# Optimization experiments

Hardware: AMD Instinct MI355X
Metric: run time of the kernel (lower is better)

The kernel has to match this reference:

```python
import jax, jax.numpy as jnp
import numpy as np

B, T = 64, 200
NUM_C2 = 2000
NUM_D = 1000
V = 128

# NOTE: Dropout layers are identity in eval mode; this reference implements eval-mode forward.

def setup_inputs() -> dict:
    key = jax.random.key(0)
    ks = jax.random.split(key, 19)
    s = 0.05
    def nrm(k, shape):
        return jax.random.normal(k, shape, jnp.float32) * s
    return {
        "c_seq": jax.random.randint(ks[0], (B, T), 0, NUM_C2),
        "d_seq": jax.random.randint(ks[1], (B, T), 0, NUM_D),
        "r_seq": (jax.random.uniform(ks[2], (B, T)) < 0.5).astype(jnp.float32),
        "D_emb": nrm(ks[3], (NUM_D, 1)),
        "v_d": nrm(ks[4], (V,)),
        "v_r": nrm(ks[5], (V,)),
        "v_c": nrm(ks[6], (V,)),
        "W_ih": nrm(ks[7], (3 * V, 2 * V)),
        "W_hh": nrm(ks[8], (3 * V, V)),
        "b_ih": nrm(ks[9], (3 * V,)),
        "b_hh": nrm(ks[10], (3 * V,)),
        "W1a": nrm(ks[11], (V, V)),
        "b1a": nrm(ks[12], (V,)),
        "W1b": nrm(ks[13], (1, V)),
        "b1b": nrm(ks[14], (1,)),
        "W2a": nrm(ks[15], (V, 3 * V)),
        "b2a": nrm(ks[16], (V,)),
        "W2b": nrm(ks[17], (1, V)),
        "b2b": nrm(ks[18], (1,)),
    }


def reference(c_seq, d_seq, r_seq, D_emb, v_d, v_r, v_c,
              W_ih, W_hh, b_ih, b_hh, W1a, b1a, W1b, b1b,
              W2a, b2a, W2b, b2b):
    gamma_seq = D_emb[d_seq]                 # [B,T,1]
    v_d_seq = gamma_seq * v_d                # [B,T,V]
    v_r_seq = r_seq[..., None] * v_r         # [B,T,V]
    x = jnp.concatenate([v_d_seq, v_r_seq], axis=-1)  # [B,T,2V]

    # --- GRU (PyTorch gate ordering r,z,n), h0 = 0 ---
    def gru_step(h, x_t):
        gi = x_t @ W_ih.T + b_ih
        gh = h @ W_hh.T + b_hh
        i_r, i_z, i_n = jnp.split(gi, 3, axis=-1)
        h_r, h_z, h_n = jnp.split(gh, 3, axis=-1)
        r = jax.nn.sigmoid(i_r + h_r)
        z = jax.nn.sigmoid(i_z + h_z)
        n = jnp.tanh(i_n + r * h_n)
        h_new = (1.0 - z) * n + z * h
        return h_new, h_new

    h0 = jnp.zeros((c_seq.shape[0], v_d.shape[0]), x.dtype)
    _, h_seq = jax.lax.scan(gru_step, h0, jnp.swapaxes(x, 0, 1))
    h_seq = jnp.swapaxes(h_seq, 0, 1)        # [B,T,V]

    # linear_1 (dropout = identity in eval)
    alpha_seq = (jax.nn.relu(h_seq @ W1a.T + b1a) @ W1b.T + b1b)[..., 0]  # [B,T]

    # --- sequential memory update over time ---
    def mem_step(C, inputs):
        c_t, vd_t, vr_t = inputs             # [B], [B,V], [B,V]
        beta = jnp.take_along_axis(C, c_t[:, None], axis=1)   # [B,1]
        vc = beta * v_c                       # [B,V]
        hh = jax.nn.relu(jnp.concatenate([vc, vd_t, vr_t], axis=-1) @ W2a.T + b2a)
        new_c = hh @ W2b.T + b2b              # [B,1]
        oh = jax.nn.one_hot(c_t, C.shape[1], dtype=C.dtype)   # [B,K]
        C_new = C * (1.0 - oh) + new_c * oh
        return C_new, C_new

    C0 = jnp.zeros((c_seq.shape[0], NUM_C2), x.dtype)
    _, C_seq = jax.lax.scan(
        mem_step, C0,
        (jnp.swapaxes(c_seq, 0, 1), jnp.swapaxes(v_d_seq, 0, 1), jnp.swapaxes(v_r_seq, 0, 1)))
    C_seq = jnp.swapaxes(C_seq, 0, 1)[..., None]   # [B,T,K,1]
    return alpha_seq, h_seq, C_seq
```

## Files before the change

### kernel.cpp

```cpp
#include <hip/hip_runtime.h>
#include <hip/hip_bf16.h>
#include <cstdint>

#define BB 64
#define TT 200
#define KN 2000
#define VV 128
#define NGRU 16

typedef __attribute__((ext_vector_type(8))) short bf16x8;
typedef __attribute__((ext_vector_type(4))) float f32x4;
typedef _Float16 half8 __attribute__((ext_vector_type(8)));


__device__ __forceinline__ float sigm(float x) {
    return __builtin_amdgcn_rcpf(1.f + __expf(-x));
}
__device__ __forceinline__ float tanh_f(float x) {
    float e = __expf(2.f * x);
    return 1.f - 2.f * __builtin_amdgcn_rcpf(e + 1.f);
}

__device__ __forceinline__ void soft_barrier() {
    asm volatile("s_waitcnt lgkmcnt(0)" ::: "memory");
    __builtin_amdgcn_s_barrier();
    __builtin_amdgcn_sched_barrier(0);
}

__global__ void pre_kernel(const float* __restrict__ v_d, const float* __restrict__ v_r,
                           const float* __restrict__ v_c, const float* __restrict__ W_ih,
                           const float* __restrict__ W2a, float* __restrict__ ws)
{
    int g = blockIdx.x * 256 + threadIdx.x;
    float* pd = ws;
    float* pr = ws + 384;
    float* uc = ws + 768;
    float* ud = ws + 896;
    float* ur = ws + 1024;
    if (g < 384) {
        float a = 0.f, b = 0.f;
        for (int k = 0; k < VV; ++k) {
            a = fmaf(W_ih[g * 256 + k], v_d[k], a);
            b = fmaf(W_ih[g * 256 + VV + k], v_r[k], b);
        }
        pd[g] = a; pr[g] = b;
    }
    if (g < VV) {
        float a = 0.f, b = 0.f, c = 0.f;
        for (int k = 0; k < VV; ++k) {
            a = fmaf(W2a[g * 384 + k], v_c[k], a);
            b = fmaf(W2a[g * 384 + VV + k], v_d[k], b);
            c = fmaf(W2a[g * 384 + 2 * VV + k], v_r[k], c);
        }
        uc[g] = a; ud[g] = b; ur[g] = c;
    }
}

__device__ __forceinline__ half8 load_cvt8h(const float* p) {
    float4 a = *(const float4*)p;
    float4 c = *(const float4*)(p + 4);
    half8 r;
    r[0] = (_Float16)a.x; r[1] = (_Float16)a.y; r[2] = (_Float16)a.z; r[3] = (_Float16)a.w;
    r[4] = (_Float16)c.x; r[5] = (_Float16)c.y; r[6] = (_Float16)c.z; r[7] = (_Float16)c.w;
    return r;
}

__global__ __launch_bounds__(512, 1) void fused_kernel(
    const int* __restrict__ c_seq, const int* __restrict__ d_seq,
    const float* __restrict__ r_seq, const float* __restrict__ D_emb,
    const float* __restrict__ Whh, const float* __restrict__ bih,
    const float* __restrict__ bhh, const float* __restrict__ W2b,
    const float* __restrict__ b2a, const float* __restrict__ b2b,
    const float* __restrict__ ws, float* __restrict__ C_out,
    float* __restrict__ h_out)
{
    __shared__ __align__(16) _Float16 H_half[16 * 136];
    __shared__ __align__(8) float gam4[TT * 4], r4[TT * 4];
    __shared__ __align__(16) float C[KN];
    __shared__ float gam_row[TT], r_row[TT], n_row[TT];
    __shared__ int c_row[TT + 1];

    int tid = threadIdx.x;

    if (blockIdx.x < NGRU) {
        int b0 = blockIdx.x * 4;
        const float* pd = ws;
        const float* pr = ws + 384;

        for (int i = tid; i < TT * 4; i += 512) {
            int t = i >> 2, rr = i & 3;
            gam4[i] = D_emb[d_seq[(b0 + rr) * TT + t]];
            r4[i] = r_seq[(b0 + rr) * TT + t];
        }
        for (int i = tid; i < 16 * 136; i += 512) H_half[i] = (_Float16)0.f;

        int wid = tid >> 6, l = tid & 63;
        int cl = l & 15, gq = l >> 4;
        int nn = wid * 16 + cl;

        const float* wr = Whh + (size_t)nn * VV + gq * 8;
        const float* wz = Whh + (size_t)(nn + 128) * VV + gq * 8;
        const float* wn = Whh + (size_t)(nn + 256) * VV + gq * 8;
        half8 br0 = load_cvt8h(wr),      br1 = load_cvt8h(wr + 32),
              br2 = load_cvt8h(wr + 64), br3 = load_cvt8h(wr + 96);
        half8 bz0 = load_cvt8h(wz),      bz1 = load_cvt8h(wz + 32),
              bz2 = load_cvt8h(wz + 64), bz3 = load_cvt8h(wz + 96);
        half8 bn0 = load_cvt8h(wn),      bn1 = load_cvt8h(wn + 32),
              bn2 = load_cvt8h(wn + 64), bn3 = load_cvt8h(wn + 96);

        float gr_pd = pd[nn],        gr_pr = pr[nn],        gr_b = bih[nn] + bhh[nn];
        float gz_pd = pd[nn + 128],  gz_pr = pr[nn + 128],  gz_b = bih[nn + 128] + bhh[nn + 128];
        float gn_pd = pd[nn + 256],  gn_pr = pr[nn + 256],  gn_b = bih[nn + 256];
        float gn_bh = bhh[nn + 256];

        float h0 = 0.f;
        __syncthreads();

        for (int t = 0; t < TT; ++t) {
            asm volatile("" : "+v"(br0), "+v"(br1), "+v"(br2), "+v"(br3),
                              "+v"(bz0), "+v"(bz1), "+v"(bz2), "+v"(bz3),
                              "+v"(bn0), "+v"(bn1), "+v"(bn2), "+v"(bn3));
            const int ab = cl * 136 + gq * 8;
            half8 a0 = *(const half8*)&H_half[ab];
            half8 a1 = *(const half8*)&H_half[ab + 32];
            half8 a2 = *(const half8*)&H_half[ab + 64];
            half8 a3 = *(const half8*)&H_half[ab + 96];
            float g1 = gam4[t * 4 + gq];
            float q1 = r4[t * 4 + gq];

            f32x4 accr = {0.f, 0.f, 0.f, 0.f};
            f32x4 accz = {0.f, 0.f, 0.f, 0.f};
            f32x4 accn = {0.f, 0.f, 0.f, 0.f};
            accr[0] = fmaf(g1, gr_pd, fmaf(q1, gr_pr, gr_b));
            accz[0] = fmaf(g1, gz_pd, fmaf(q1, gz_pr, gz_b));
            accn[0] = gn_bh;
            float gin0 = fmaf(g1, gn_pd, fmaf(q1, gn_pr, gn_b));

            accr = __builtin_amdgcn_mfma_f32_16x16x32_f16(a0, br0, accr, 0, 0, 0);
            accr = __builtin_amdgcn_mfma_f32_16x16x32_f16(a1, br1, accr, 0, 0, 0);
            accr = __builtin_amdgcn_mfma_f32_16x16x32_f16(a2, br2, accr, 0, 0, 0);
            accr = __builtin_amdgcn_mfma_f32_16x16x32_f16(a3, br3, accr, 0, 0, 0);
            accz = __builtin_amdgcn_mfma_f32_16x16x32_f16(a0, bz0, accz, 0, 0, 0);
            accz = __builtin_amdgcn_mfma_f32_16x16x32_f16(a1, bz1, accz, 0, 0, 0);
            accz = __builtin_amdgcn_mfma_f32_16x16x32_f16(a2, bz2, accz, 0, 0, 0);
            accz = __builtin_amdgcn_mfma_f32_16x16x32_f16(a3, bz3, accz, 0, 0, 0);
            accn = __builtin_amdgcn_mfma_f32_16x16x32_f16(a0, bn0, accn, 0, 0, 0);
            accn = __builtin_amdgcn_mfma_f32_16x16x32_f16(a1, bn1, accn, 0, 0, 0);
            accn = __builtin_amdgcn_mfma_f32_16x16x32_f16(a2, bn2, accn, 0, 0, 0);
            accn = __builtin_amdgcn_mfma_f32_16x16x32_f16(a3, bn3, accn, 0, 0, 0);

            {
                float rg0 = sigm(accr[0]);
                float zg0 = sigm(accz[0]);
                float ng0 = tanh_f(fmaf(rg0, accn[0], gin0));
                h0 = fmaf(1.f - zg0, ng0, zg0 * h0);
                h_out[((size_t)(b0 + gq) * TT + t) * VV + nn] = h0;
                H_half[(gq * 4) * 136 + nn] = (_Float16)h0;
            }
            soft_barrier();
        }
    } else {
        int b = blockIdx.x - NGRU;
        const float* uc = ws + 768;
        const float* ud = ws + 896;
        const float* ur = ws + 1024;
        for (int i = tid; i < KN; i += 512) C[i] = 0.f;
        if (tid < TT) {
            gam_row[tid] = D_emb[d_seq[b * TT + tid]];
            r_row[tid] = r_seq[b * TT + tid];
            c_row[tid] = c_seq[b * TT + tid];
        }
        if (tid == 0) c_row[TT] = 0;
        __syncthreads();

        if (tid < 64) {
            int l = tid;
            float uc0 = uc[l], uc1 = uc[l + 64];
            float ud0 = ud[l], ud1 = ud[l + 64];
            float ur0 = ur[l], ur1 = ur[l + 64];
            float ba0 = b2a[l], ba1 = b2a[l + 64];
            float wb0 = W2b[l], wb1 = W2b[l + 64];
            float bb = b2b[0];
            float beta = 0.f;
            int ct = c_row[0];
            for (int t = 0; t < TT; ++t) {
                int ct1 = c_row[t + 1];
                float cpref = C[ct1];
                float g = gam_row[t], rr = r_row[t];
                float hh0 = fmaxf(fmaf(beta, uc0, fmaf(g, ud0, fmaf(rr, ur0, ba0))), 0.f);
                float hh1 = fmaxf(fmaf(beta, uc1, fmaf(g, ud1, fmaf(rr, ur1, ba1))), 0.f);
                float p = fmaf(hh0, wb0, hh1 * wb1);
                #pragma unroll
                for (int m = 32; m > 0; m >>= 1) p += __shfl_xor(p, m);
                float nc = p + bb;
                if (l == 0) { C[ct] = nc; n_row[t] = nc; }
                beta = (ct1 == ct) ? nc : cpref;
                ct = ct1;
            }
        }
        __syncthreads();

        int k0 = tid * 4;
        if (k0 < KN) {
            float4 cur = {0.f, 0.f, 0.f, 0.f};
            float* cop = C_out + (size_t)b * TT * KN + k0;
            for (int t = 0; t < TT; ++t) {
                int c = c_row[t];
                unsigned d = (unsigned)(c - k0);
                if (d < 4u) {
                    float v = n_row[t];
                    cur.x = (d == 0u) ? v : cur.x;
                    cur.y = (d == 1u) ? v : cur.y;
                    cur.z = (d == 2u) ? v : cur.z;
                    cur.w = (d == 3u) ? v : cur.w;
                }
                *(float4*)(cop + (size_t)t * KN) = cur;
            }
        }
    }
}

__device__ __forceinline__ short f2bf(float f) {
    uint32_t u = __float_as_uint(f);
    u = (u + 0x7FFFu + ((u >> 16) & 1u)) >> 16;
    return (short)u;
}
__device__ __forceinline__ bf16x8 load_cvt8(const float* p) {
    float4 a = *(const float4*)p;
    float4 c = *(const float4*)(p + 4);
    bf16x8 r;
    r[0] = f2bf(a.x); r[1] = f2bf(a.y); r[2] = f2bf(a.z); r[3] = f2bf(a.w);
    r[4] = f2bf(c.x); r[5] = f2bf(c.y); r[6] = f2bf(c.z); r[7] = f2bf(c.w);
    return r;
}

__global__ void alpha_kernel(const float* __restrict__ h_seq, const float* __restrict__ W1a,
                             const float* __restrict__ b1a, const float* __restrict__ W1b,
                             const float* __restrict__ b1b, float* __restrict__ alpha)
{
    int wave = threadIdx.x >> 6;
    int lane = threadIdx.x & 63;
    int tile = blockIdx.x * 4 + wave;
    int rowbase = tile * 16;
    int rl = lane & 15, g = lane >> 4;
    const float* hp = h_seq + (size_t)(rowbase + rl) * VV + g * 8;
    bf16x8 a0 = load_cvt8(hp);
    bf16x8 a1 = load_cvt8(hp + 32);
    bf16x8 a2 = load_cvt8(hp + 64);
    bf16x8 a3 = load_cvt8(hp + 96);
    float p0 = 0.f, p1 = 0.f, p2 = 0.f, p3 = 0.f;
    float bb = b1b[0];
    #pragma unroll
    for (int jt = 0; jt < 8; ++jt) {
        int j = jt * 16 + rl;
        const float* wp = W1a + (size_t)j * VV + g * 8;
        f32x4 acc = {0.f, 0.f, 0.f, 0.f};
        acc = __builtin_amdgcn_mfma_f32_16x16x32_bf16(a0, load_cvt8(wp), acc, 0, 0, 0);
        acc = __builtin_amdgcn_mfma_f32_16x16x32_bf16(a1, load_cvt8(wp + 32), acc, 0, 0, 0);
        acc = __builtin_amdgcn_mfma_f32_16x16x32_bf16(a2, load_cvt8(wp + 64), acc, 0, 0, 0);
        acc = __builtin_amdgcn_mfma_f32_16x16x32_bf16(a3, load_cvt8(wp + 96), acc, 0, 0, 0);
        float bj = b1a[j], wj = W1b[j];
        p0 += fmaxf(acc[0] + bj, 0.f) * wj;
        p1 += fmaxf(acc[1] + bj, 0.f) * wj;
        p2 += fmaxf(acc[2] + bj, 0.f) * wj;
        p3 += fmaxf(acc[3] + bj, 0.f) * wj;
    }
    #pragma unroll
    for (int m = 1; m < 16; m <<= 1) {
        p0 += __shfl_xor(p0, m);
        p1 += __shfl_xor(p1, m);
        p2 += __shfl_xor(p2, m);
        p3 += __shfl_xor(p3, m);
    }
    if (rl == 0) {
        alpha[rowbase + g * 4 + 0] = p0 + bb;
        alpha[rowbase + g * 4 + 1] = p1 + bb;
        alpha[rowbase + g * 4 + 2] = p2 + bb;
        alpha[rowbase + g * 4 + 3] = p3 + bb;
    }
}

extern "C" void kernel_launch(void* const* d_in, const int* in_sizes, int n_in,
                              void* d_out, int out_size, void* d_ws, size_t ws_size,
                              hipStream_t stream)
{
    const int*   c_seq = (const int*)d_in[0];
    const int*   d_seq = (const int*)d_in[1];
    const float* r_seq = (const float*)d_in[2];
    const float* D_emb = (const float*)d_in[3];
    const float* v_d   = (const float*)d_in[4];
    const float* v_r   = (const float*)d_in[5];
    const float* v_c   = (const float*)d_in[6];
    const float* W_ih  = (const float*)d_in[7];
    const float* W_hh  = (const float*)d_in[8];
    const float* b_ih  = (const float*)d_in[9];
    const float* b_hh  = (const float*)d_in[10];
    const float* W1a   = (const float*)d_in[11];
    const float* b1a   = (const float*)d_in[12];
    const float* W1b   = (const float*)d_in[13];
    const float* b1b   = (const float*)d_in[14];
    const float* W2a   = (const float*)d_in[15];
    const float* b2a   = (const float*)d_in[16];
    const float* W2b   = (const float*)d_in[17];
    const float* b2b   = (const float*)d_in[18];

    float* out   = (float*)d_out;
    float* alpha = out;
    float* h_seq = out + 12800;
    float* C_out = out + 12800 + 1638400;
    float* ws    = (float*)d_ws;

    hipLaunchKernelGGL(pre_kernel, dim3(2), dim3(256), 0, stream,
                       v_d, v_r, v_c, W_ih, W2a, ws);
    hipLaunchKernelGGL(fused_kernel, dim3(NGRU + BB), dim3(512), 0, stream,
                       c_seq, d_seq, r_seq, D_emb, W_hh, b_ih, b_hh,
                       W2b, b2a, b2b, ws, C_out, h_seq);
    hipLaunchKernelGGL(alpha_kernel, dim3(200), dim3(256), 0, stream,
                       h_seq, W1a, b1a, W1b, b1b, alpha);
}
```

Measured before the change: 120.8 us.

## Fold precompute into fused kernel, use counter-based group sync, stage W1a in LDS

Removes the separate pre_kernel launch and has each block compute its W_ih and W2a projections inline. GRU blocks become 1024 threads carrying two independent 4-batch groups, with double-buffered hidden state and a per-group LDS atomic counter replacing the block-wide barrier. Memory blocks go to 1024 threads writing C in float2 chunks. The alpha kernel now stages W1a as bf16 in shared memory and runs 8 waves per block. The intent is to cut launch overhead and barrier cost. The trade-offs are redundant dot products in every block and spin-wait overhead.

```diff
diff --git a/kernel.cpp b/kernel.cpp
--- a/kernel.cpp
+++ b/kernel.cpp
@@ -6,13 +6,12 @@
 #define TT 200
 #define KN 2000
 #define VV 128
-#define NGRU 16
+#define NGRU 8
 
 typedef __attribute__((ext_vector_type(8))) short bf16x8;
 typedef __attribute__((ext_vector_type(4))) float f32x4;
 typedef _Float16 half8 __attribute__((ext_vector_type(8)));
 
-
 __device__ __forceinline__ float sigm(float x) {
     return __builtin_amdgcn_rcpf(1.f + __expf(-x));
 }
@@ -21,39 +20,17 @@
     return 1.f - 2.f * __builtin_amdgcn_rcpf(e + 1.f);
 }
 
-__device__ __forceinline__ void soft_barrier() {
-    asm volatile("s_waitcnt lgkmcnt(0)" ::: "memory");
-    __builtin_amdgcn_s_barrier();
-    __builtin_amdgcn_sched_barrier(0);
-}
-
-__global__ void pre_kernel(const float* __restrict__ v_d, const float* __restrict__ v_r,
-                           const float* __restrict__ v_c, const float* __restrict__ W_ih,
-                           const float* __restrict__ W2a, float* __restrict__ ws)
-{
-    int g = blockIdx.x * 256 + threadIdx.x;
-    float* pd = ws;
-    float* pr = ws + 384;
-    float* uc = ws + 768;
-    float* ud = ws + 896;
-    float* ur = ws + 1024;
-    if (g < 384) {
-        float a = 0.f, b = 0.f;
-        for (int k = 0; k < VV; ++k) {
-            a = fmaf(W_ih[g * 256 + k], v_d[k], a);
-            b = fmaf(W_ih[g * 256 + VV + k], v_r[k], b);
-        }
-        pd[g] = a; pr[g] = b;
-    }
-    if (g < VV) {
-        float a = 0.f, b = 0.f, c = 0.f;
-        for (int k = 0; k < VV; ++k) {
-            a = fmaf(W2a[g * 384 + k], v_c[k], a);
-            b = fmaf(W2a[g * 384 + VV + k], v_d[k], b);
-            c = fmaf(W2a[g * 384 + 2 * VV + k], v_r[k], c);
-        }
-        uc[g] = a; ud[g] = b; ur[g] = c;
-    }
+__device__ __forceinline__ float dot128(const float* __restrict__ a,
+                                        const float* __restrict__ b) {
+    float s0 = 0.f, s1 = 0.f, s2 = 0.f, s3 = 0.f;
+    #pragma unroll 8
+    for (int k = 0; k < 128; k += 4) {
+        float4 x = *(const float4*)(a + k);
+        float4 y = *(const float4*)(b + k);
+        s0 = fmaf(x.x, y.x, s0); s1 = fmaf(x.y, y.y, s1);
+        s2 = fmaf(x.z, y.z, s2); s3 = fmaf(x.w, y.w, s3);
+    }
+    return (s0 + s1) + (s2 + s3);
 }
 
 __device__ __forceinline__ half8 load_cvt8h(const float* p) {
@@ -65,17 +42,20 @@
     return r;
 }
 
-__global__ __launch_bounds__(512, 1) void fused_kernel(
+__global__ __launch_bounds__(1024, 1) void fused_kernel(
     const int* __restrict__ c_seq, const int* __restrict__ d_seq,
     const float* __restrict__ r_seq, const float* __restrict__ D_emb,
-    const float* __restrict__ Whh, const float* __restrict__ bih,
-    const float* __restrict__ bhh, const float* __restrict__ W2b,
-    const float* __restrict__ b2a, const float* __restrict__ b2b,
-    const float* __restrict__ ws, float* __restrict__ C_out,
+    const float* __restrict__ W_ih, const float* __restrict__ Whh,
+    const float* __restrict__ bih, const float* __restrict__ bhh,
+    const float* __restrict__ v_d, const float* __restrict__ v_r,
+    const float* __restrict__ v_c, const float* __restrict__ W2a,
+    const float* __restrict__ W2b, const float* __restrict__ b2a,
+    const float* __restrict__ b2b, float* __restrict__ C_out,
     float* __restrict__ h_out)
 {
-    __shared__ __align__(16) _Float16 H_half[16 * 136];
-    __shared__ __align__(8) float gam4[TT * 4], r4[TT * 4];
+    __shared__ __align__(16) _Float16 Hbuf[2][2][16 * 136];
+    __shared__ __align__(8) float gam4[2][TT * 4], r4[2][TT * 4];
+    __shared__ unsigned cnt[2];
     __shared__ __align__(16) float C[KN];
     __shared__ float gam_row[TT], r_row[TT], n_row[TT];
     __shared__ int c_row[TT + 1];
@@ -83,20 +63,24 @@
     int tid = threadIdx.x;
 
     if (blockIdx.x < NGRU) {
-        int b0 = blockIdx.x * 4;
-        const float* pd = ws;
-        const float* pr = ws + 384;
-
-        for (int i = tid; i < TT * 4; i += 512) {
-            int t = i >> 2, rr = i & 3;
-            gam4[i] = D_emb[d_seq[(b0 + rr) * TT + t]];
-            r4[i] = r_seq[(b0 + rr) * TT + t];
-        }
-        for (int i = tid; i < 16 * 136; i += 512) H_half[i] = (_Float16)0.f;
-
         int wid = tid >> 6, l = tid & 63;
+        int g = wid >> 3, wg = wid & 7;
         int cl = l & 15, gq = l >> 4;
-        int nn = wid * 16 + cl;
+        int nn = wg * 16 + cl;
+        int b0g = blockIdx.x * 8 + g * 4;
+        int brow = b0g + gq;
+
+        for (int i = tid; i < TT * 8; i += 1024) {
+            int grp = i >= TT * 4;
+            int w = i - grp * TT * 4;
+            int t = w >> 2, rr = w & 3;
+            int bb_ = blockIdx.x * 8 + grp * 4 + rr;
+            gam4[grp][t * 4 + rr] = D_emb[d_seq[bb_ * TT + t]];
+            r4[grp][t * 4 + rr] = r_seq[bb_ * TT + t];
+        }
+        for (int i = tid; i < 2 * 2 * 16 * 136; i += 1024)
+            ((_Float16*)Hbuf)[i] = (_Float16)0.f;
+        if (tid < 2) cnt[tid] = 0u;
 
         const float* wr = Whh + (size_t)nn * VV + gq * 8;
         const float* wz = Whh + (size_t)(nn + 128) * VV + gq * 8;
@@ -108,9 +92,15 @@
         half8 bn0 = load_cvt8h(wn),      bn1 = load_cvt8h(wn + 32),
               bn2 = load_cvt8h(wn + 64), bn3 = load_cvt8h(wn + 96);
 
-        float gr_pd = pd[nn],        gr_pr = pr[nn],        gr_b = bih[nn] + bhh[nn];
-        float gz_pd = pd[nn + 128],  gz_pr = pr[nn + 128],  gz_b = bih[nn + 128] + bhh[nn + 128];
-        float gn_pd = pd[nn + 256],  gn_pr = pr[nn + 256],  gn_b = bih[nn + 256];
+        float gr_pd = dot128(W_ih + (size_t)nn * 256, v_d);
+        float gr_pr = dot128(W_ih + (size_t)nn * 256 + 128, v_r);
+        float gz_pd = dot128(W_ih + (size_t)(nn + 128) * 256, v_d);
+        float gz_pr = dot128(W_ih + (size_t)(nn + 128) * 256 + 128, v_r);
+        float gn_pd = dot128(W_ih + (size_t)(nn + 256) * 256, v_d);
+        float gn_pr = dot128(W_ih + (size_t)(nn + 256) * 256 + 128, v_r);
+        float gr_b = bih[nn] + bhh[nn];
+        float gz_b = bih[nn + 128] + bhh[nn + 128];
+        float gn_b = bih[nn + 256];
         float gn_bh = bhh[nn + 256];
 
         float h0 = 0.f;
@@ -120,13 +110,16 @@
             asm volatile("" : "+v"(br0), "+v"(br1), "+v"(br2), "+v"(br3),
                               "+v"(bz0), "+v"(bz1), "+v"(bz2), "+v"(bz3),
                               "+v"(bn0), "+v"(bn1), "+v"(bn2), "+v"(bn3));
+            const _Float16* Hr = Hbuf[g][t & 1];
+            _Float16* Hw = Hbuf[g][(t & 1) ^ 1];
+
             const int ab = cl * 136 + gq * 8;
-            half8 a0 = *(const half8*)&H_half[ab];
-            half8 a1 = *(const half8*)&H_half[ab + 32];
-            half8 a2 = *(const half8*)&H_half[ab + 64];
-            half8 a3 = *(const half8*)&H_half[ab + 96];
-            float g1 = gam4[t * 4 + gq];
-            float q1 = r4[t * 4 + gq];
+            half8 a0 = *(const half8*)&Hr[ab];
+            half8 a1 = *(const half8*)&Hr[ab + 32];
+            half8 a2 = *(const half8*)&Hr[ab + 64];
+            half8 a3 = *(const half8*)&Hr[ab + 96];
+            float g1 = gam4[g][t * 4 + gq];
+            float q1 = r4[g][t * 4 + gq];
 
             f32x4 accr = {0.f, 0.f, 0.f, 0.f};
             f32x4 accz = {0.f, 0.f, 0.f, 0.f};
@@ -154,33 +147,46 @@
                 float zg0 = sigm(accz[0]);
                 float ng0 = tanh_f(fmaf(rg0, accn[0], gin0));
                 h0 = fmaf(1.f - zg0, ng0, zg0 * h0);
-                h_out[((size_t)(b0 + gq) * TT + t) * VV + nn] = h0;
-                H_half[(gq * 4) * 136 + nn] = (_Float16)h0;
+                h_out[((size_t)brow * TT + t) * VV + nn] = h0;
+                Hw[(gq * 4) * 136 + nn] = (_Float16)h0;
             }
-            soft_barrier();
+
+            asm volatile("s_waitcnt lgkmcnt(0)" ::: "memory");
+            if (l == 0)
+                __hip_atomic_fetch_add(&cnt[g], 1u, __ATOMIC_RELEASE,
+                                       __HIP_MEMORY_SCOPE_WORKGROUP);
+            unsigned tgt = 8u * (unsigned)(t + 1);
+            while (__hip_atomic_load(&cnt[g], __ATOMIC_ACQUIRE,
+                                     __HIP_MEMORY_SCOPE_WORKGROUP) < tgt) {}
+            __builtin_amdgcn_sched_barrier(0);
         }
     } else {
         int b = blockIdx.x - NGRU;
-        const float* uc = ws + 768;
-        const float* ud = ws + 896;
-        const float* ur = ws + 1024;
-        for (int i = tid; i < KN; i += 512) C[i] = 0.f;
+        for (int i = tid; i < KN; i += 1024) C[i] = 0.f;
         if (tid < TT) {
             gam_row[tid] = D_emb[d_seq[b * TT + tid]];
             r_row[tid] = r_seq[b * TT + tid];
             c_row[tid] = c_seq[b * TT + tid];
         }
         if (tid == 0) c_row[TT] = 0;
-        __syncthreads();
-
+        float uc0 = 0.f, uc1 = 0.f, ud0 = 0.f, ud1 = 0.f, ur0 = 0.f, ur1 = 0.f;
+        float ba0 = 0.f, ba1 = 0.f, wb0 = 0.f, wb1 = 0.f, bb = 0.f;
         if (tid < 64) {
             int l = tid;
-            float uc0 = uc[l], uc1 = uc[l + 64];
-            float ud0 = ud[l], ud1 = ud[l + 64];
-            float ur0 = ur[l], ur1 = ur[l + 64];
-            float ba0 = b2a[l], ba1 = b2a[l + 64];
-            float wb0 = W2b[l], wb1 = W2b[l + 64];
-            float bb = b2b[0];
+            uc0 = dot128(W2a + (size_t)l * 384, v_c);
+            ud0 = dot128(W2a + (size_t)l * 384 + 128, v_d);
+            ur0 = dot128(W2a + (size_t)l * 384 + 256, v_r);
+            uc1 = dot128(W2a + (size_t)(l + 64) * 384, v_c);
+            ud1 = dot128(W2a + (size_t)(l + 64) * 384 + 128, v_d);
+            ur1 = dot128(W2a + (size_t)(l + 64) * 384 + 256, v_r);
+            ba0 = b2a[l]; ba1 = b2a[l + 64];
+            wb0 = W2b[l]; wb1 = W2b[l + 64];
+            bb = b2b[0];
+        }
+        __syncthreads();
+
+        if (tid < 64) {
+            int l = tid;
             float beta = 0.f;
             int ct = c_row[0];
             for (int t = 0; t < TT; ++t) {
@@ -200,21 +206,19 @@
         }
         __syncthreads();
 
-        int k0 = tid * 4;
+        int k0 = tid * 2;
         if (k0 < KN) {
-            float4 cur = {0.f, 0.f, 0.f, 0.f};
+            float2 cur = {0.f, 0.f};
             float* cop = C_out + (size_t)b * TT * KN + k0;
             for (int t = 0; t < TT; ++t) {
                 int c = c_row[t];
                 unsigned d = (unsigned)(c - k0);
-                if (d < 4u) {
+                if (d < 2u) {
                     float v = n_row[t];
                     cur.x = (d == 0u) ? v : cur.x;
                     cur.y = (d == 1u) ? v : cur.y;
-                    cur.z = (d == 2u) ? v : cur.z;
-                    cur.w = (d == 3u) ? v : cur.w;
                 }
-                *(float4*)(cop + (size_t)t * KN) = cur;
+                *(float2*)(cop + (size_t)t * KN) = cur;
             }
         }
     }
@@ -234,13 +238,23 @@
     return r;
 }
 
-__global__ void alpha_kernel(const float* __restrict__ h_seq, const float* __restrict__ W1a,
-                             const float* __restrict__ b1a, const float* __restrict__ W1b,
-                             const float* __restrict__ b1b, float* __restrict__ alpha)
+__global__ __launch_bounds__(512) void alpha_kernel(
+    const float* __restrict__ h_seq, const float* __restrict__ W1a,
+    const float* __restrict__ b1a, const float* __restrict__ W1b,
+    const float* __restrict__ b1b, float* __restrict__ alpha)
 {
-    int wave = threadIdx.x >> 6;
-    int lane = threadIdx.x & 63;
-    int tile = blockIdx.x * 4 + wave;
+    __shared__ __align__(16) short W1s[128 * 136];
+    __shared__ float b1s[128], w1bs[128];
+    int tid = threadIdx.x;
+    for (int i = tid * 8; i < 128 * 128; i += 512 * 8) {
+        int row = i >> 7, col = i & 127;
+        *(bf16x8*)&W1s[row * 136 + col] = load_cvt8(W1a + i);
+    }
+    if (tid < 128) { b1s[tid] = b1a[tid]; w1bs[tid] = W1b[tid]; }
+    __syncthreads();
+
+    int wave = tid >> 6, lane = tid & 63;
+    int tile = blockIdx.x * 8 + wave;
     int rowbase = tile * 16;
     int rl = lane & 15, g = lane >> 4;
     const float* hp = h_seq + (size_t)(rowbase + rl) * VV + g * 8;
@@ -253,13 +267,13 @@
     #pragma unroll
     for (int jt = 0; jt < 8; ++jt) {
         int j = jt * 16 + rl;
-        const float* wp = W1a + (size_t)j * VV + g * 8;
+        const short* wp = &W1s[j * 136 + g * 8];
         f32x4 acc = {0.f, 0.f, 0.f, 0.f};
-        acc = __builtin_amdgcn_mfma_f32_16x16x32_bf16(a0, load_cvt8(wp), acc, 0, 0, 0);
-        acc = __builtin_amdgcn_mfma_f32_16x16x32_bf16(a1, load_cvt8(wp + 32), acc, 0, 0, 0);
-        acc = __builtin_amdgcn_mfma_f32_16x16x32_bf16(a2, load_cvt8(wp + 64), acc, 0, 0, 0);
-        acc = __builtin_amdgcn_mfma_f32_16x16x32_bf16(a3, load_cvt8(wp + 96), acc, 0, 0, 0);
-        float bj = b1a[j], wj = W1b[j];
+        acc = __builtin_amdgcn_mfma_f32_16x16x32_bf16(a0, *(const bf16x8*)wp, acc, 0, 0, 0);
+        acc = __builtin_amdgcn_mfma_f32_16x16x32_bf16(a1, *(const bf16x8*)(wp + 32), acc, 0, 0, 0);
+        acc = __builtin_amdgcn_mfma_f32_16x16x32_bf16(a2, *(const bf16x8*)(wp + 64), acc, 0, 0, 0);
+        acc = __builtin_amdgcn_mfma_f32_16x16x32_bf16(a3, *(const bf16x8*)(wp + 96), acc, 0, 0, 0);
+        float bj = b1s[j], wj = w1bs[j];
         p0 += fmaxf(acc[0] + bj, 0.f) * wj;
         p1 += fmaxf(acc[1] + bj, 0.f) * wj;
         p2 += fmaxf(acc[2] + bj, 0.f) * wj;
@@ -308,13 +322,10 @@
     float* alpha = out;
     float* h_seq = out + 12800;
     float* C_out = out + 12800 + 1638400;
-    float* ws    = (float*)d_ws;
-
-    hipLaunchKernelGGL(pre_kernel, dim3(2), dim3(256), 0, stream,
-                       v_d, v_r, v_c, W_ih, W2a, ws);
-    hipLaunchKernelGGL(fused_kernel, dim3(NGRU + BB), dim3(512), 0, stream,
-                       c_seq, d_seq, r_seq, D_emb, W_hh, b_ih, b_hh,
-                       W2b, b2a, b2b, ws, C_out, h_seq);
-    hipLaunchKernelGGL(alpha_kernel, dim3(200), dim3(256), 0, stream,
+
+    hipLaunchKernelGGL(fused_kernel, dim3(NGRU + BB), dim3(1024), 0, stream,
+                       c_seq, d_seq, r_seq, D_emb, W_ih, W_hh, b_ih, b_hh,
+                       v_d, v_r, v_c, W2a, W2b, b2a, b2b, C_out, h_seq);
+    hipLaunchKernelGGL(alpha_kernel, dim3(100), dim3(512), 0, stream,
                        h_seq, W1a, b1a, W1b, b1b, alpha);
 }
```

New measurement: 242.1 us. 100% more time.
